# Kernel optimization log

Measured on AMD Instinct MI355X. Metric: run time of the kernel, lower is better.

Reference implementation:

```python
import jax, jax.numpy as jnp
import numpy as np

D_MODEL = 768
N_HEADS = 12
D_HEAD = D_MODEL // N_HEADS


def setup_inputs() -> dict:
    key = jax.random.key(0)
    ks = jax.random.split(key, 6)
    B, T = 2, 4096
    x = jax.random.normal(ks[0], (B, T, D_MODEL), dtype=jnp.float32)
    mask = jnp.ones((B, T), dtype=jnp.int32)
    # torch nn.Linear: weight [out, in], bias [out]
    s_in = 1.0 / np.sqrt(D_MODEL)
    w_qkv = jax.random.uniform(ks[1], (3 * D_MODEL, D_MODEL), jnp.float32, -s_in, s_in)
    b_qkv = jax.random.uniform(ks[2], (3 * D_MODEL,), jnp.float32, -s_in, s_in)
    w_out = jax.random.uniform(ks[3], (D_MODEL, D_MODEL), jnp.float32, -s_in, s_in)
    b_out = jax.random.uniform(ks[4], (D_MODEL,), jnp.float32, -s_in, s_in)
    return {"x": x, "w_qkv": w_qkv, "b_qkv": b_qkv, "w_out": w_out, "b_out": b_out, "mask": mask}


def reference(x, w_qkv, b_qkv, w_out, b_out, mask):
    B, T, C = x.shape
    # fused QKV projection: [B,T,3C]
    qkv = x @ w_qkv.T + b_qkv
    qkv = qkv.reshape(B, T, 3, N_HEADS, D_HEAD)
    qkv = jnp.transpose(qkv, (2, 0, 3, 1, 4))  # [3,B,H,T,Dh]
    q, k, v = qkv[0], qkv[1], qkv[2]
    scale = jnp.float32(np.sqrt(D_HEAD))
    scores = jnp.einsum('bhqd,bhkd->bhqk', q, k) / scale  # [B,H,T,T]
    scores = jnp.where(mask[:, None, None, :] == 0, jnp.float32(-1e9), scores)
    weights = jax.nn.softmax(scores, axis=-1)  # dropout p=0 (eval-mode reference)
    out = jnp.einsum('bhqk,bhkd->bhqd', weights, v)  # [B,H,T,Dh]
    out = jnp.transpose(out, (0, 2, 1, 3)).reshape(B, T, C)
    return out @ w_out.T + b_out
```

## Files before the change

### kernel.cpp

```cpp
#include <hip/hip_runtime.h>
#include <hip/hip_bf16.h>
#include <cstdint>
#include <cstddef>

#define D_MODEL 768
#define N_HEADS 12
#define T_SEQ   4096
#define B_BATCH 2
#define BT      (B_BATCH * T_SEQ)

typedef __attribute__((ext_vector_type(8))) short bf16x8;
typedef __attribute__((ext_vector_type(4))) float f32x4;

__device__ __forceinline__ short fbf(float f) {
  __hip_bfloat16 h = __float2bfloat16(f);
  return __builtin_bit_cast(short, h);
}

__device__ __forceinline__ void gl_lds16(const void* g, void* l) {
  __builtin_amdgcn_global_load_lds(
      (const __attribute__((address_space(1))) void*)g,
      (__attribute__((address_space(3))) void*)l, 16, 0, 0);
}

__global__ __launch_bounds__(256) void cast_bf16(const float* __restrict__ in,
                                                 short* __restrict__ out, int n8) {
  int i = blockIdx.x * 256 + threadIdx.x;
  if (i >= n8) return;
  const float4* p = (const float4*)in + (size_t)i * 2;
  float4 v0 = p[0], v1 = p[1];
  bf16x8 o;
  o[0] = fbf(v0.x); o[1] = fbf(v0.y); o[2] = fbf(v0.z); o[3] = fbf(v0.w);
  o[4] = fbf(v1.x); o[5] = fbf(v1.y); o[6] = fbf(v1.z); o[7] = fbf(v1.w);
  *(bf16x8*)(out + (size_t)i * 8) = o;
}

__global__ __launch_bounds__(256) void mask_count(const int* __restrict__ mask,
                                                  float* __restrict__ nm) {
  __shared__ int red[256];
  int s = 0;
  for (int i = threadIdx.x; i < T_SEQ; i += 256) s += mask[blockIdx.x * T_SEQ + i];
  red[threadIdx.x] = s;
  __syncthreads();
  for (int off = 128; off > 0; off >>= 1) {
    if (threadIdx.x < off) red[threadIdx.x] += red[threadIdx.x + off];
    __syncthreads();
  }
  if (threadIdx.x == 0) nm[blockIdx.x] = (float)(T_SEQ - red[0]);
}

template<int EPI>
__global__ __launch_bounds__(256) void gemm_bt(
    const short* __restrict__ A, const short* __restrict__ Bm,
    const float* __restrict__ bias, int K, int N,
    short* __restrict__ Qb, short* __restrict__ Kb, short* __restrict__ Vt,
    const int* __restrict__ maskp, float* __restrict__ Cout)
{
  __shared__ __align__(16) short smem[128 * 132];
  short* As = smem;
  short* Bs = smem + 128 * 64;
  typedef short CtRow[132];
  CtRow* Ct = (CtRow*)smem;

  const int t = threadIdx.x;
  const int lane = t & 63, wave = t >> 6;
  const int a = lane & 15, g = lane >> 4;
  const int wr = wave >> 1, wc = wave & 1;
  const int bm = blockIdx.x * 128, bn = blockIdx.y * 128;

  f32x4 acc[4][4];
  #pragma unroll
  for (int i = 0; i < 4; ++i)
    #pragma unroll
    for (int j = 0; j < 4; ++j) acc[i][j] = f32x4{0.f, 0.f, 0.f, 0.f};

  const int nkt = K >> 6;
  for (int kt = 0; kt < nkt; ++kt) {
    const int k0 = kt << 6;
    __syncthreads();
    #pragma unroll
    for (int it = 0; it < 4; ++it) {
      int cid = it * 256 + t;
      int row = cid >> 3, c16 = cid & 7;
      int sc = c16 ^ (row & 7);
      gl_lds16(A  + (size_t)(bm + row) * K + k0 + sc * 8, (char*)As + (it * 256 + wave * 64) * 16);
      gl_lds16(Bm + (size_t)(bn + row) * K + k0 + sc * 8, (char*)Bs + (it * 256 + wave * 64) * 16);
    }
    __syncthreads();
    #pragma unroll
    for (int c = 0; c < 2; ++c) {
      bf16x8 af[4], bfr[4];
      #pragma unroll
      for (int mi = 0; mi < 4; ++mi) {
        int row = wr * 64 + mi * 16 + a;
        af[mi] = *(const bf16x8*)((const char*)As + row * 128 + ((c * 64 + g * 16) ^ ((row & 7) << 4)));
      }
      #pragma unroll
      for (int ni = 0; ni < 4; ++ni) {
        int row = wc * 64 + ni * 16 + a;
        bfr[ni] = *(const bf16x8*)((const char*)Bs + row * 128 + ((c * 64 + g * 16) ^ ((row & 7) << 4)));
      }
      #pragma unroll
      for (int mi = 0; mi < 4; ++mi)
        #pragma unroll
        for (int ni = 0; ni < 4; ++ni)
          acc[mi][ni] = __builtin_amdgcn_mfma_f32_16x16x32_bf16(af[mi], bfr[ni], acc[mi][ni], 0, 0, 0);
    }
  }

  if (EPI == 1) {
    #pragma unroll
    for (int mi = 0; mi < 4; ++mi) {
      int rowb = bm + wr * 64 + mi * 16 + g * 4;
      #pragma unroll
      for (int ni = 0; ni < 4; ++ni) {
        int col = bn + wc * 64 + ni * 16 + a;
        float bv = bias[col];
        #pragma unroll
        for (int r = 0; r < 4; ++r)
          Cout[(size_t)(rowb + r) * N + col] = acc[mi][ni][r] + bv;
      }
    }
  } else {
    const float QSCALE = 0.125f * 1.44269504088896f;
    const int sec = bn / D_MODEL;
    const int bb = bm >> 12, tt0 = bm & 4095;
    if (sec < 2) {
      #pragma unroll
      for (int ni = 0; ni < 4; ++ni) {
        int n = bn + wc * 64 + ni * 16 + a;
        int wcol = n - sec * D_MODEL;
        int h = wcol >> 6, d = wcol & 63;
        float bv = bias[n];
        size_t bhoff = (size_t)(bb * N_HEADS + h);
        #pragma unroll
        for (int mi = 0; mi < 4; ++mi) {
          #pragma unroll
          for (int r = 0; r < 4; ++r) {
            int tt = tt0 + wr * 64 + mi * 16 + g * 4 + r;
            float val = acc[mi][ni][r] + bv;
            if (sec == 0) Qb[(bhoff * T_SEQ + tt) * 64 + d] = fbf(val * QSCALE);
            else          Kb[(bhoff * T_SEQ + tt) * 64 + d] =
                              fbf(val * (float)maskp[(size_t)bb * T_SEQ + tt]);
          }
        }
      }
    } else {
      __syncthreads();
      #pragma unroll
      for (int ni = 0; ni < 4; ++ni) {
        int col_t = wc * 64 + ni * 16 + a;
        float bv = bias[bn + col_t];
        #pragma unroll
        for (int mi = 0; mi < 4; ++mi) {
          #pragma unroll
          for (int r = 0; r < 4; ++r) {
            int rowin = wr * 64 + mi * 16 + g * 4 + r;
            int tt = tt0 + rowin;
            float val = (acc[mi][ni][r] + bv) * (float)maskp[(size_t)bb * T_SEQ + tt];
            int t6 = rowin & 63;
            int rowp = (rowin & 64) | (((t6 >> 4) & 1) << 5) | (((t6 >> 2) & 3) << 3)
                     | (((t6 >> 5) & 1) << 2) | (t6 & 3);
            Ct[col_t][rowp] = fbf(val);
          }
        }
      }
      __syncthreads();
      const int wb = bn - 2 * D_MODEL;
      #pragma unroll
      for (int it = 0; it < 32; ++it) {
        int col = wave * 32 + it;
        int wcol = wb + col;
        int h = wcol >> 6, d = wcol & 63;
        size_t base = ((size_t)(bb * N_HEADS + h) * 64 + d) * T_SEQ + tt0;
        *(short2*)(Vt + base + 2 * lane) = *(const short2*)&Ct[col][2 * lane];
      }
    }
  }
}

__global__ __launch_bounds__(256, 3) void attn(
    const short* __restrict__ Qb, const short* __restrict__ Kb, const short* __restrict__ Vt,
    const float* __restrict__ nmasked, short* __restrict__ Ao)
{
  __shared__ __align__(16) short KV[3][2][64 * 64];

  const int t = threadIdx.x;
  const int lane = t & 63, wave = t >> 6;
  const int a = lane & 15, g = lane >> 4;

  const int flat = blockIdx.x;
  const int xcd = flat & 7, slot = flat >> 3;
  const int logical = xcd * 96 + slot;
  const int bh = logical >> 5;
  const int qblk = logical & 31;

  const int b = bh / N_HEADS, h = bh - b * N_HEADS;
  const size_t headoff = (size_t)bh * T_SEQ * 64;
  const int q0 = qblk * 128 + wave * 32;

  const int srow0 = t >> 3, sc0 = (t & 7) ^ (srow0 & 7);
  const int srow1 = (256 + t) >> 3, sc1 = (t & 7) ^ (srow1 & 7);
  const short* Kh = Kb + headoff;
  const short* Vh = Vt + headoff;
  const float nm = nmasked[b];

  bf16x8 qf[2][2];
  #pragma unroll
  for (int qg = 0; qg < 2; ++qg) {
    const short* qrow = Qb + headoff + (size_t)(q0 + qg * 16 + a) * 64;
    qf[qg][0] = *(const bf16x8*)(qrow + g * 8);
    qf[qg][1] = *(const bf16x8*)(qrow + 32 + g * 8);
  }

  bf16x8 ones;
  #pragma unroll
  for (int i = 0; i < 8; ++i) ones[i] = (short)0x3F80;

  int foff[2][4];
  #pragma unroll
  for (int c = 0; c < 2; ++c)
    #pragma unroll
    for (int ni = 0; ni < 4; ++ni) {
      int row = ni * 16 + a;
      foff[c][ni] = row * 128 + ((c * 64 + g * 16) ^ ((row & 7) << 4));
    }

  f32x4 o[2][4];
  f32x4 ladd[2];
  #pragma unroll
  for (int qg = 0; qg < 2; ++qg) {
    ladd[qg] = f32x4{0.f, 0.f, 0.f, 0.f};
    #pragma unroll
    for (int i = 0; i < 4; ++i) o[qg][i] = f32x4{0.f, 0.f, 0.f, 0.f};
  }

#define STAGE(buf, kb)                                                                        \
  do {                                                                                        \
    gl_lds16(Kh + (size_t)((kb) + srow0) * 64 + sc0 * 8,  (char*)KV[buf][0] + (wave * 64) * 16);       \
    gl_lds16(Vh + (size_t)srow0 * T_SEQ + (kb) + sc0 * 8, (char*)KV[buf][1] + (wave * 64) * 16);       \
    gl_lds16(Kh + (size_t)((kb) + srow1) * 64 + sc1 * 8,  (char*)KV[buf][0] + (256 + wave * 64) * 16); \
    gl_lds16(Vh + (size_t)srow1 * T_SEQ + (kb) + sc1 * 8, (char*)KV[buf][1] + (256 + wave * 64) * 16); \
  } while (0)

  STAGE(0, 0);
  STAGE(1, 64);

  const int NT = T_SEQ / 64;
  int cur = 0, nx2 = 2;
  for (int kt = 0; kt < NT; ++kt) {
    if (kt < NT - 1) asm volatile("s_waitcnt vmcnt(4)" ::: "memory");
    else             asm volatile("s_waitcnt vmcnt(0)" ::: "memory");
    __builtin_amdgcn_s_barrier();
    if (kt + 2 < NT) STAGE(nx2, (kt + 2) * 64);

    const char* Ktc = (const char*)KV[cur][0];
    const char* Vsc = (const char*)KV[cur][1];

    f32x4 st[2][4];
    #pragma unroll
    for (int qg = 0; qg < 2; ++qg)
      #pragma unroll
      for (int ni = 0; ni < 4; ++ni) st[qg][ni] = f32x4{0.f,0.f,0.f,0.f};

    __builtin_amdgcn_s_setprio(1);
    #pragma unroll
    for (int c = 0; c < 2; ++c) {
      #pragma unroll
      for (int ni = 0; ni < 4; ++ni) {
        bf16x8 kf = *(const bf16x8*)(Ktc + foff[c][ni]);
        st[0][ni] = __builtin_amdgcn_mfma_f32_16x16x32_bf16(kf, qf[0][c], st[0][ni], 0, 0, 0);
        st[1][ni] = __builtin_amdgcn_mfma_f32_16x16x32_bf16(kf, qf[1][c], st[1][ni], 0, 0, 0);
      }
    }
    __builtin_amdgcn_s_setprio(0);

    bf16x8 pa[2][2];
    #pragma unroll
    for (int qg = 0; qg < 2; ++qg)
      #pragma unroll
      for (int ni = 0; ni < 4; ++ni) {
        const int c = ni & 1, jb = (ni >> 1) * 4;
        #pragma unroll
        for (int r = 0; r < 4; ++r)
          pa[qg][c][jb + r] = fbf(__builtin_amdgcn_exp2f(st[qg][ni][r]));
      }

    __builtin_amdgcn_s_setprio(1);
    #pragma unroll
    for (int c = 0; c < 2; ++c) {
      ladd[0] = __builtin_amdgcn_mfma_f32_16x16x32_bf16(pa[0][c], ones, ladd[0], 0, 0, 0);
      ladd[1] = __builtin_amdgcn_mfma_f32_16x16x32_bf16(pa[1][c], ones, ladd[1], 0, 0, 0);
      #pragma unroll
      for (int di = 0; di < 4; ++di) {
        bf16x8 vf = *(const bf16x8*)(Vsc + foff[c][di]);
        o[0][di] = __builtin_amdgcn_mfma_f32_16x16x32_bf16(pa[0][c], vf, o[0][di], 0, 0, 0);
        o[1][di] = __builtin_amdgcn_mfma_f32_16x16x32_bf16(pa[1][c], vf, o[1][di], 0, 0, 0);
      }
    }
    __builtin_amdgcn_s_setprio(0);

    cur = cur + 1; if (cur == 3) cur = 0;
    nx2 = nx2 + 1; if (nx2 == 3) nx2 = 0;
  }
#undef STAGE

  #pragma unroll
  for (int qg = 0; qg < 2; ++qg) {
    float linv[4];
    #pragma unroll
    for (int r = 0; r < 4; ++r) linv[r] = 1.f / (ladd[qg][r] - nm);
    #pragma unroll
    for (int di = 0; di < 4; ++di)
      #pragma unroll
      for (int r = 0; r < 4; ++r) {
        int rowg = b * T_SEQ + q0 + qg * 16 + g * 4 + r;
        Ao[(size_t)rowg * D_MODEL + h * 64 + di * 16 + a] = fbf(o[qg][di][r] * linv[r]);
      }
  }
}

extern "C" void kernel_launch(void* const* d_in, const int* in_sizes, int n_in,
                              void* d_out, int out_size, void* d_ws, size_t ws_size,
                              hipStream_t stream) {
  const float* x     = (const float*)d_in[0];
  const float* w_qkv = (const float*)d_in[1];
  const float* b_qkv = (const float*)d_in[2];
  const float* w_out = (const float*)d_in[3];
  const float* b_out = (const float*)d_in[4];
  const int*   mask  = (const int*)d_in[5];
  float* out = (float*)d_out;

  char* w = (char*)d_ws;
  short* xb    = (short*)w; w += (size_t)BT * D_MODEL * 2;
  short* wqkvb = (short*)w; w += (size_t)3 * D_MODEL * D_MODEL * 2;
  short* woutb = (short*)w; w += (size_t)D_MODEL * D_MODEL * 2;
  short* Qb    = (short*)w; w += (size_t)BT * D_MODEL * 2;
  short* Kb    = (short*)w; w += (size_t)BT * D_MODEL * 2;
  short* Vt    = (short*)w; w += (size_t)BT * D_MODEL * 2;
  short* Ao    = (short*)w; w += (size_t)BT * D_MODEL * 2;
  float* nm    = (float*)w; w += 2 * sizeof(float);

  {
    int n8 = BT * D_MODEL / 8;
    cast_bf16<<<n8 / 256, 256, 0, stream>>>(x, xb, n8);
  }
  {
    int n8 = 3 * D_MODEL * D_MODEL / 8;
    cast_bf16<<<n8 / 256, 256, 0, stream>>>(w_qkv, wqkvb, n8);
  }
  {
    int n8 = D_MODEL * D_MODEL / 8;
    cast_bf16<<<n8 / 256, 256, 0, stream>>>(w_out, woutb, n8);
  }
  mask_count<<<2, 256, 0, stream>>>(mask, nm);

  gemm_bt<0><<<dim3(BT / 128, 3 * D_MODEL / 128), 256, 0, stream>>>(
      xb, wqkvb, b_qkv, D_MODEL, 3 * D_MODEL, Qb, Kb, Vt, mask, nullptr);

  attn<<<768, 256, 0, stream>>>(Qb, Kb, Vt, nm, Ao);

  gemm_bt<1><<<dim3(BT / 128, D_MODEL / 128), 256, 0, stream>>>(
      Ao, woutb, b_out, D_MODEL, D_MODEL, nullptr, nullptr, nullptr, nullptr, out);
}
```

Measured before the change: 255.8 us.

## Split attention across 8 waves, fuse prep kernels, shrink output GEMM tile

The attention kernel now runs 512 threads per block with 8 waves, each handling 16 query rows instead of 32. The K/V staging is spread over more threads, so each thread issues fewer loads, and per-wave register use drops. The three casts and the mask count are merged into one prep launch to cut launch overhead. The output projection GEMM uses 64-row tiles to double its block count and fill more CUs. The cost is that each K/V tile in LDS is reused by fewer query rows per wave, and more waves must share each barrier.

```diff
diff --git a/kernel.cpp b/kernel.cpp
--- a/kernel.cpp
+++ b/kernel.cpp
@@ -23,54 +23,64 @@
       (__attribute__((address_space(3))) void*)l, 16, 0, 0);
 }
 
-__global__ __launch_bounds__(256) void cast_bf16(const float* __restrict__ in,
-                                                 short* __restrict__ out, int n8) {
-  int i = blockIdx.x * 256 + threadIdx.x;
-  if (i >= n8) return;
-  const float4* p = (const float4*)in + (size_t)i * 2;
-  float4 v0 = p[0], v1 = p[1];
-  bf16x8 o;
-  o[0] = fbf(v0.x); o[1] = fbf(v0.y); o[2] = fbf(v0.z); o[3] = fbf(v0.w);
-  o[4] = fbf(v1.x); o[5] = fbf(v1.y); o[6] = fbf(v1.z); o[7] = fbf(v1.w);
-  *(bf16x8*)(out + (size_t)i * 8) = o;
-}
-
-__global__ __launch_bounds__(256) void mask_count(const int* __restrict__ mask,
-                                                  float* __restrict__ nm) {
+__global__ __launch_bounds__(256) void prep(
+    const float* __restrict__ x, const float* __restrict__ wqkv,
+    const float* __restrict__ wout, const int* __restrict__ mask,
+    short* __restrict__ xb, short* __restrict__ wqkvb, short* __restrict__ woutb,
+    float* __restrict__ nm)
+{
   __shared__ int red[256];
-  int s = 0;
-  for (int i = threadIdx.x; i < T_SEQ; i += 256) s += mask[blockIdx.x * T_SEQ + i];
-  red[threadIdx.x] = s;
-  __syncthreads();
-  for (int off = 128; off > 0; off >>= 1) {
-    if (threadIdx.x < off) red[threadIdx.x] += red[threadIdx.x + off];
+  const int B0 = 3072, B1 = 3936, B2 = 4224;
+  int blk = blockIdx.x;
+  if (blk < B2) {
+    const float* in; short* out; int i;
+    if (blk < B0)      { in = x;    out = xb;    i = blk * 256 + threadIdx.x; }
+    else if (blk < B1) { in = wqkv; out = wqkvb; i = (blk - B0) * 256 + threadIdx.x; }
+    else               { in = wout; out = woutb; i = (blk - B1) * 256 + threadIdx.x; }
+    const float4* p = (const float4*)in + (size_t)i * 2;
+    float4 v0 = p[0], v1 = p[1];
+    bf16x8 o;
+    o[0] = fbf(v0.x); o[1] = fbf(v0.y); o[2] = fbf(v0.z); o[3] = fbf(v0.w);
+    o[4] = fbf(v1.x); o[5] = fbf(v1.y); o[6] = fbf(v1.z); o[7] = fbf(v1.w);
+    *(bf16x8*)(out + (size_t)i * 8) = o;
+  } else {
+    int b = blk - B2;
+    int s = 0;
+    for (int i = threadIdx.x; i < T_SEQ; i += 256) s += mask[b * T_SEQ + i];
+    red[threadIdx.x] = s;
     __syncthreads();
-  }
-  if (threadIdx.x == 0) nm[blockIdx.x] = (float)(T_SEQ - red[0]);
-}
-
-template<int EPI>
+    for (int off = 128; off > 0; off >>= 1) {
+      if (threadIdx.x < off) red[threadIdx.x] += red[threadIdx.x + off];
+      __syncthreads();
+    }
+    if (threadIdx.x == 0) nm[b] = (float)(T_SEQ - red[0]);
+  }
+}
+
+template<int EPI, int TM>
 __global__ __launch_bounds__(256) void gemm_bt(
     const short* __restrict__ A, const short* __restrict__ Bm,
     const float* __restrict__ bias, int K, int N,
     short* __restrict__ Qb, short* __restrict__ Kb, short* __restrict__ Vt,
     const int* __restrict__ maskp, float* __restrict__ Cout)
 {
-  __shared__ __align__(16) short smem[128 * 132];
+  constexpr int SMEM = (EPI == 0) ? 128 * 132 : (TM * 64 + 128 * 64);
+  __shared__ __align__(16) short smem[SMEM];
   short* As = smem;
-  short* Bs = smem + 128 * 64;
+  short* Bs = smem + TM * 64;
   typedef short CtRow[132];
   CtRow* Ct = (CtRow*)smem;
 
+  constexpr int MI = TM / 32;
   const int t = threadIdx.x;
   const int lane = t & 63, wave = t >> 6;
   const int a = lane & 15, g = lane >> 4;
   const int wr = wave >> 1, wc = wave & 1;
-  const int bm = blockIdx.x * 128, bn = blockIdx.y * 128;
-
-  f32x4 acc[4][4];
-  #pragma unroll
-  for (int i = 0; i < 4; ++i)
+  const int bm = blockIdx.x * TM, bn = blockIdx.y * 128;
+
+  f32x4 acc[MI][4];
+  #pragma unroll
+  for (int i = 0; i < MI; ++i)
     #pragma unroll
     for (int j = 0; j < 4; ++j) acc[i][j] = f32x4{0.f, 0.f, 0.f, 0.f};
 
@@ -79,20 +89,24 @@
     const int k0 = kt << 6;
     __syncthreads();
     #pragma unroll
+    for (int it = 0; it < TM / 32; ++it) {
+      int cid = it * 256 + t;
+      int row = cid >> 3, c16 = cid & 7, sc = c16 ^ (row & 7);
+      gl_lds16(A + (size_t)(bm + row) * K + k0 + sc * 8, (char*)As + (it * 256 + wave * 64) * 16);
+    }
+    #pragma unroll
     for (int it = 0; it < 4; ++it) {
       int cid = it * 256 + t;
-      int row = cid >> 3, c16 = cid & 7;
-      int sc = c16 ^ (row & 7);
-      gl_lds16(A  + (size_t)(bm + row) * K + k0 + sc * 8, (char*)As + (it * 256 + wave * 64) * 16);
+      int row = cid >> 3, c16 = cid & 7, sc = c16 ^ (row & 7);
       gl_lds16(Bm + (size_t)(bn + row) * K + k0 + sc * 8, (char*)Bs + (it * 256 + wave * 64) * 16);
     }
     __syncthreads();
     #pragma unroll
     for (int c = 0; c < 2; ++c) {
-      bf16x8 af[4], bfr[4];
-      #pragma unroll
-      for (int mi = 0; mi < 4; ++mi) {
-        int row = wr * 64 + mi * 16 + a;
+      bf16x8 af[MI], bfr[4];
+      #pragma unroll
+      for (int mi = 0; mi < MI; ++mi) {
+        int row = wr * (TM / 2) + mi * 16 + a;
         af[mi] = *(const bf16x8*)((const char*)As + row * 128 + ((c * 64 + g * 16) ^ ((row & 7) << 4)));
       }
       #pragma unroll
@@ -101,7 +115,7 @@
         bfr[ni] = *(const bf16x8*)((const char*)Bs + row * 128 + ((c * 64 + g * 16) ^ ((row & 7) << 4)));
       }
       #pragma unroll
-      for (int mi = 0; mi < 4; ++mi)
+      for (int mi = 0; mi < MI; ++mi)
         #pragma unroll
         for (int ni = 0; ni < 4; ++ni)
           acc[mi][ni] = __builtin_amdgcn_mfma_f32_16x16x32_bf16(af[mi], bfr[ni], acc[mi][ni], 0, 0, 0);
@@ -110,8 +124,8 @@
 
   if (EPI == 1) {
     #pragma unroll
-    for (int mi = 0; mi < 4; ++mi) {
-      int rowb = bm + wr * 64 + mi * 16 + g * 4;
+    for (int mi = 0; mi < MI; ++mi) {
+      int rowb = bm + wr * (TM / 2) + mi * 16 + g * 4;
       #pragma unroll
       for (int ni = 0; ni < 4; ++ni) {
         int col = bn + wc * 64 + ni * 16 + a;
@@ -134,10 +148,10 @@
         float bv = bias[n];
         size_t bhoff = (size_t)(bb * N_HEADS + h);
         #pragma unroll
-        for (int mi = 0; mi < 4; ++mi) {
+        for (int mi = 0; mi < MI; ++mi) {
           #pragma unroll
           for (int r = 0; r < 4; ++r) {
-            int tt = tt0 + wr * 64 + mi * 16 + g * 4 + r;
+            int tt = tt0 + wr * (TM / 2) + mi * 16 + g * 4 + r;
             float val = acc[mi][ni][r] + bv;
             if (sec == 0) Qb[(bhoff * T_SEQ + tt) * 64 + d] = fbf(val * QSCALE);
             else          Kb[(bhoff * T_SEQ + tt) * 64 + d] =
@@ -152,10 +166,10 @@
         int col_t = wc * 64 + ni * 16 + a;
         float bv = bias[bn + col_t];
         #pragma unroll
-        for (int mi = 0; mi < 4; ++mi) {
+        for (int mi = 0; mi < MI; ++mi) {
           #pragma unroll
           for (int r = 0; r < 4; ++r) {
-            int rowin = wr * 64 + mi * 16 + g * 4 + r;
+            int rowin = wr * (TM / 2) + mi * 16 + g * 4 + r;
             int tt = tt0 + rowin;
             float val = (acc[mi][ni][r] + bv) * (float)maskp[(size_t)bb * T_SEQ + tt];
             int t6 = rowin & 63;
@@ -179,7 +193,7 @@
   }
 }
 
-__global__ __launch_bounds__(256, 3) void attn(
+__global__ __launch_bounds__(512, 6) void attn(
     const short* __restrict__ Qb, const short* __restrict__ Kb, const short* __restrict__ Vt,
     const float* __restrict__ nmasked, short* __restrict__ Ao)
 {
@@ -197,20 +211,18 @@
 
   const int b = bh / N_HEADS, h = bh - b * N_HEADS;
   const size_t headoff = (size_t)bh * T_SEQ * 64;
-  const int q0 = qblk * 128 + wave * 32;
-
-  const int srow0 = t >> 3, sc0 = (t & 7) ^ (srow0 & 7);
-  const int srow1 = (256 + t) >> 3, sc1 = (t & 7) ^ (srow1 & 7);
+  const int q0 = qblk * 128 + wave * 16;
+
+  const int srow = t >> 3, sc = (t & 7) ^ (srow & 7);
   const short* Kh = Kb + headoff;
   const short* Vh = Vt + headoff;
   const float nm = nmasked[b];
 
-  bf16x8 qf[2][2];
-  #pragma unroll
-  for (int qg = 0; qg < 2; ++qg) {
-    const short* qrow = Qb + headoff + (size_t)(q0 + qg * 16 + a) * 64;
-    qf[qg][0] = *(const bf16x8*)(qrow + g * 8);
-    qf[qg][1] = *(const bf16x8*)(qrow + 32 + g * 8);
+  bf16x8 qf[2];
+  {
+    const short* qrow = Qb + headoff + (size_t)(q0 + a) * 64;
+    qf[0] = *(const bf16x8*)(qrow + g * 8);
+    qf[1] = *(const bf16x8*)(qrow + 32 + g * 8);
   }
 
   bf16x8 ones;
@@ -226,21 +238,15 @@
       foff[c][ni] = row * 128 + ((c * 64 + g * 16) ^ ((row & 7) << 4));
     }
 
-  f32x4 o[2][4];
-  f32x4 ladd[2];
-  #pragma unroll
-  for (int qg = 0; qg < 2; ++qg) {
-    ladd[qg] = f32x4{0.f, 0.f, 0.f, 0.f};
-    #pragma unroll
-    for (int i = 0; i < 4; ++i) o[qg][i] = f32x4{0.f, 0.f, 0.f, 0.f};
-  }
-
-#define STAGE(buf, kb)                                                                        \
-  do {                                                                                        \
-    gl_lds16(Kh + (size_t)((kb) + srow0) * 64 + sc0 * 8,  (char*)KV[buf][0] + (wave * 64) * 16);       \
-    gl_lds16(Vh + (size_t)srow0 * T_SEQ + (kb) + sc0 * 8, (char*)KV[buf][1] + (wave * 64) * 16);       \
-    gl_lds16(Kh + (size_t)((kb) + srow1) * 64 + sc1 * 8,  (char*)KV[buf][0] + (256 + wave * 64) * 16); \
-    gl_lds16(Vh + (size_t)srow1 * T_SEQ + (kb) + sc1 * 8, (char*)KV[buf][1] + (256 + wave * 64) * 16); \
+  f32x4 o[4];
+  f32x4 ladd = f32x4{0.f, 0.f, 0.f, 0.f};
+  #pragma unroll
+  for (int i = 0; i < 4; ++i) o[i] = f32x4{0.f, 0.f, 0.f, 0.f};
+
+#define STAGE(buf, kb)                                                                  \
+  do {                                                                                  \
+    gl_lds16(Kh + (size_t)((kb) + srow) * 64 + sc * 8,  (char*)KV[buf][0] + wave * 1024); \
+    gl_lds16(Vh + (size_t)srow * T_SEQ + (kb) + sc * 8, (char*)KV[buf][1] + wave * 1024); \
   } while (0)
 
   STAGE(0, 0);
@@ -249,7 +255,7 @@
   const int NT = T_SEQ / 64;
   int cur = 0, nx2 = 2;
   for (int kt = 0; kt < NT; ++kt) {
-    if (kt < NT - 1) asm volatile("s_waitcnt vmcnt(4)" ::: "memory");
+    if (kt < NT - 1) asm volatile("s_waitcnt vmcnt(2)" ::: "memory");
     else             asm volatile("s_waitcnt vmcnt(0)" ::: "memory");
     __builtin_amdgcn_s_barrier();
     if (kt + 2 < NT) STAGE(nx2, (kt + 2) * 64);
@@ -257,11 +263,9 @@
     const char* Ktc = (const char*)KV[cur][0];
     const char* Vsc = (const char*)KV[cur][1];
 
-    f32x4 st[2][4];
-    #pragma unroll
-    for (int qg = 0; qg < 2; ++qg)
-      #pragma unroll
-      for (int ni = 0; ni < 4; ++ni) st[qg][ni] = f32x4{0.f,0.f,0.f,0.f};
+    f32x4 st[4];
+    #pragma unroll
+    for (int ni = 0; ni < 4; ++ni) st[ni] = f32x4{0.f,0.f,0.f,0.f};
 
     __builtin_amdgcn_s_setprio(1);
     #pragma unroll
@@ -269,33 +273,28 @@
       #pragma unroll
       for (int ni = 0; ni < 4; ++ni) {
         bf16x8 kf = *(const bf16x8*)(Ktc + foff[c][ni]);
-        st[0][ni] = __builtin_amdgcn_mfma_f32_16x16x32_bf16(kf, qf[0][c], st[0][ni], 0, 0, 0);
-        st[1][ni] = __builtin_amdgcn_mfma_f32_16x16x32_bf16(kf, qf[1][c], st[1][ni], 0, 0, 0);
+        st[ni] = __builtin_amdgcn_mfma_f32_16x16x32_bf16(kf, qf[c], st[ni], 0, 0, 0);
       }
     }
     __builtin_amdgcn_s_setprio(0);
 
-    bf16x8 pa[2][2];
-    #pragma unroll
-    for (int qg = 0; qg < 2; ++qg)
-      #pragma unroll
-      for (int ni = 0; ni < 4; ++ni) {
-        const int c = ni & 1, jb = (ni >> 1) * 4;
-        #pragma unroll
-        for (int r = 0; r < 4; ++r)
-          pa[qg][c][jb + r] = fbf(__builtin_amdgcn_exp2f(st[qg][ni][r]));
-      }
+    bf16x8 pa[2];
+    #pragma unroll
+    for (int ni = 0; ni < 4; ++ni) {
+      const int c = ni & 1, jb = (ni >> 1) * 4;
+      #pragma unroll
+      for (int r = 0; r < 4; ++r)
+        pa[c][jb + r] = fbf(__builtin_amdgcn_exp2f(st[ni][r]));
+    }
 
     __builtin_amdgcn_s_setprio(1);
     #pragma unroll
     for (int c = 0; c < 2; ++c) {
-      ladd[0] = __builtin_amdgcn_mfma_f32_16x16x32_bf16(pa[0][c], ones, ladd[0], 0, 0, 0);
-      ladd[1] = __builtin_amdgcn_mfma_f32_16x16x32_bf16(pa[1][c], ones, ladd[1], 0, 0, 0);
+      ladd = __builtin_amdgcn_mfma_f32_16x16x32_bf16(pa[c], ones, ladd, 0, 0, 0);
       #pragma unroll
       for (int di = 0; di < 4; ++di) {
         bf16x8 vf = *(const bf16x8*)(Vsc + foff[c][di]);
-        o[0][di] = __builtin_amdgcn_mfma_f32_16x16x32_bf16(pa[0][c], vf, o[0][di], 0, 0, 0);
-        o[1][di] = __builtin_amdgcn_mfma_f32_16x16x32_bf16(pa[1][c], vf, o[1][di], 0, 0, 0);
+        o[di] = __builtin_amdgcn_mfma_f32_16x16x32_bf16(pa[c], vf, o[di], 0, 0, 0);
       }
     }
     __builtin_amdgcn_s_setprio(0);
@@ -305,19 +304,16 @@
   }
 #undef STAGE
 
-  #pragma unroll
-  for (int qg = 0; qg < 2; ++qg) {
-    float linv[4];
-    #pragma unroll
-    for (int r = 0; r < 4; ++r) linv[r] = 1.f / (ladd[qg][r] - nm);
-    #pragma unroll
-    for (int di = 0; di < 4; ++di)
-      #pragma unroll
-      for (int r = 0; r < 4; ++r) {
-        int rowg = b * T_SEQ + q0 + qg * 16 + g * 4 + r;
-        Ao[(size_t)rowg * D_MODEL + h * 64 + di * 16 + a] = fbf(o[qg][di][r] * linv[r]);
-      }
-  }
+  float linv[4];
+  #pragma unroll
+  for (int r = 0; r < 4; ++r) linv[r] = 1.f / (ladd[r] - nm);
+  #pragma unroll
+  for (int di = 0; di < 4; ++di)
+    #pragma unroll
+    for (int r = 0; r < 4; ++r) {
+      int rowg = b * T_SEQ + q0 + g * 4 + r;
+      Ao[(size_t)rowg * D_MODEL + h * 64 + di * 16 + a] = fbf(o[di][r] * linv[r]);
+    }
 }
 
 extern "C" void kernel_launch(void* const* d_in, const int* in_sizes, int n_in,
@@ -341,25 +337,13 @@
   short* Ao    = (short*)w; w += (size_t)BT * D_MODEL * 2;
   float* nm    = (float*)w; w += 2 * sizeof(float);
 
-  {
-    int n8 = BT * D_MODEL / 8;
-    cast_bf16<<<n8 / 256, 256, 0, stream>>>(x, xb, n8);
-  }
-  {
-    int n8 = 3 * D_MODEL * D_MODEL / 8;
-    cast_bf16<<<n8 / 256, 256, 0, stream>>>(w_qkv, wqkvb, n8);
-  }
-  {
-    int n8 = D_MODEL * D_MODEL / 8;
-    cast_bf16<<<n8 / 256, 256, 0, stream>>>(w_out, woutb, n8);
-  }
-  mask_count<<<2, 256, 0, stream>>>(mask, nm);
-
-  gemm_bt<0><<<dim3(BT / 128, 3 * D_MODEL / 128), 256, 0, stream>>>(
+  prep<<<4226, 256, 0, stream>>>(x, w_qkv, w_out, mask, xb, wqkvb, woutb, nm);
+
+  gemm_bt<0, 128><<<dim3(BT / 128, 3 * D_MODEL / 128), 256, 0, stream>>>(
       xb, wqkvb, b_qkv, D_MODEL, 3 * D_MODEL, Qb, Kb, Vt, mask, nullptr);
 
-  attn<<<768, 256, 0, stream>>>(Qb, Kb, Vt, nm, Ao);
-
-  gemm_bt<1><<<dim3(BT / 128, D_MODEL / 128), 256, 0, stream>>>(
+  attn<<<768, 512, 0, stream>>>(Qb, Kb, Vt, nm, Ao);
+
+  gemm_bt<1, 64><<<dim3(BT / 64, D_MODEL / 128), 256, 0, stream>>>(
       Ao, woutb, b_out, D_MODEL, D_MODEL, nullptr, nullptr, nullptr, nullptr, out);
 }
```

Result: no change. 255.0 us (-0.3%).
